# Kernel tuning notes

Hardware: AMD Instinct MI355X
Metric: run time of the kernel (lower is better)

The kernel has to match this reference:

```python
import jax, jax.numpy as jnp
import numpy as np

KRYLOV_DIM = 8
T_END = 1.0
EPS = 1e-12


def setup_inputs() -> dict:
    key = jax.random.key(0)
    k1, k2, k3 = jax.random.split(key, 3)
    B, C, H, Wd = 8, 256, 64, 64
    s0 = jax.random.uniform(k1, (B, C, H, Wd), dtype=jnp.float32)
    v = jax.random.normal(k2, (B, C, H, Wd), dtype=jnp.float32)
    W = jax.random.normal(k3, (C, C), dtype=jnp.float32) / np.float32(np.sqrt(C))
    return {"s0": s0, "v": v, "W": W}


def reference(s0, v, W):
    # fitness: learned channel-mixing linear operator (1x1-conv style)
    def fitness(x):
        return jnp.einsum('oc,bchw->bohw', W, x)

    # replicator vector field R_{s}[x] = s*x - s * sum_c(s*x)
    def replicator(s, x):
        sx = s * x
        return sx - s * jnp.sum(sx, axis=1, keepdims=True)

    A = lambda x: fitness(replicator(s0, x))
    dot = lambda a, b: jnp.sum(a * b, axis=(1, 2, 3))  # batched inner product

    m = KRYLOV_DIM
    B = v.shape[0]

    # ---- Arnoldi iteration (batched, modified Gram-Schmidt) ----
    vnorm = jnp.sqrt(dot(v, v))  # [B]
    Q = [v / vnorm[:, None, None, None]]
    Hcols = []
    for k in range(m):
        w = A(Q[k])
        col = []
        for j in range(k + 1):
            h = dot(Q[j], w)               # [B]
            col.append(h)
            w = w - h[:, None, None, None] * Q[j]
        hnext = jnp.sqrt(dot(w, w))        # subdiagonal entry
        Q.append(w / (hnext + EPS)[:, None, None, None])
        col.append(hnext)
        col += [jnp.zeros_like(hnext)] * (m - k - 1)  # pad column to m+1 rows
        Hcols.append(jnp.stack(col, axis=-1))          # [B, m+1]
    Hmat = jnp.stack(Hcols, axis=-1)  # [B, m+1, m]
    T = Hmat[:, :m, :]                # square upper-Hessenberg [B, m, m]

    # ---- extended matrix + batched small matrix exponential ----
    ext = jnp.zeros((B, m + 1, m + 1), dtype=T.dtype)
    ext = ext.at[:, :m, :m].set(T_END * T)
    ext = ext.at[:, 0, m].set(T_END)
    expm_ext = jax.scipy.linalg.expm(ext)   # batched over leading dim
    coords = expm_ext[:, :m, -1]            # [B, m] Krylov coordinates

    # ---- fused weighted sum of Krylov vectors ----
    Qstack = jnp.stack(Q[:m], axis=0)       # [m, B, C, H, W]
    v_end = jnp.einsum('bj,jbchw->bchw', coords, Qstack)
    return v_end * vnorm[:, None, None, None]
```

## Files before the change

### kernel.cpp

```cpp
#include <hip/hip_runtime.h>
#include <math.h>

#define Bn   8
#define Cn   256
#define HWn  4096
#define FB   (Cn * HWn)
#define NTOT (Bn * FB)
#define TEND 1.0
#define EPSK 1e-12f
#define NT   32
#define TPB  128
#define TSZ  8192
#define RS   40
#define WTS  36

typedef float f32x4 __attribute__((ext_vector_type(4)));
typedef short bf16x8 __attribute__((ext_vector_type(8)));

__device__ inline float b2f(unsigned int u) {
    return __uint_as_float(u << 16);
}
__device__ inline unsigned short f2b(float f) {
    unsigned u = __float_as_uint(f);
    unsigned r = u + 0x7FFFu + ((u >> 16) & 1u);
    return (unsigned short)(r >> 16);
}


__global__ void init_kernel(float* __restrict__ p) {
    for (int i = threadIdx.x; i < 1024; i += 256) p[i] = 0.0f;
}

__global__ void wsplit_kernel(const float* __restrict__ W,
                              unsigned short* __restrict__ Whs,
                              unsigned short* __restrict__ Wls) {
    int kc = blockIdx.x, mt = blockIdx.y, l = threadIdx.x;
    int m = mt * 16 + (l & 15);
    int k0 = kc * 32 + (l >> 4) * 8;
#pragma unroll
    for (int j = 0; j < 8; ++j) {
        float wv = W[m * 256 + k0 + j];
        unsigned short h = f2b(wv);
        unsigned short lo = f2b(wv - b2f(h));
        int idx = ((kc * 16 + mt) * 64 + l) * 8 + j;
        Whs[idx] = h; Wls[idx] = lo;
    }
}

template <int K>
__global__ __launch_bounds__(256, 2) void step_kernel(
        const float* __restrict__ v, const float* __restrict__ s0,
        const unsigned short* __restrict__ Whs, const unsigned short* __restrict__ Wls,
        unsigned short* __restrict__ Qb, float* __restrict__ acc,
        float* __restrict__ w) {
    __shared__ __align__(16) char smem_u[36864];
    short* Ph0 = (short*)smem_u;
    short* Ph1 = (short*)(smem_u + 2560);
    short* Pl0 = (short*)(smem_u + 5120);
    short* Pl1 = (short*)(smem_u + 7680);
    float* tredf = (float*)(smem_u + 10240);
    float* wt    = (float*)smem_u;
    __shared__ float ts[NT];
    __shared__ float nred[4];
    __shared__ float dred[4][8];

    const int tid = threadIdx.x;
    const int lane = tid & 63, wvi = tid >> 6;
    const int b = blockIdx.y;
    const int tIdx = blockIdx.x;
    const int sbase = tIdx * NT;
    const size_t boff = (size_t)b * FB;
    const size_t tb = ((size_t)b * TPB + tIdx) * TSZ;
    const int mbase = wvi * 64;
    const int cch = tid >> 3;
    const int pos4 = (tid & 7) * 4;
    const int codd = cch & 1;
    const int c2s = cch >> 1;

    float cj[K > 0 ? K : 1];
    if (K > 0) {
        float mm[K > 0 ? K : 1];
        mm[0] = sqrtf(acc[512 + b]);
#pragma unroll
        for (int j = 1; j < K; ++j) mm[j] = sqrtf(acc[512 + j * 8 + b]) + EPSK * mm[j - 1];
#pragma unroll
        for (int j = 0; j < K; ++j)
            cj[j] = acc[((K - 1) * 8 + j) * 8 + b] / (mm[j] * mm[j]);
    }
    unsigned short* QK = Qb + (size_t)(K > 0 ? K - 1 : 0) * NTOT;

    float tp[4] = {0.f, 0.f, 0.f, 0.f};
    float np = 0.f;
    for (int kc = 0; kc < 8; ++kc) {
        const size_t os = boff + (size_t)(kc * 32 + cch) * HWn + sbase + pos4;
        const size_t ot = tb + (size_t)((kc * 32 + cch) * NT + pos4);
        float4 s4 = *(const float4*)(s0 + os);
        float se[4] = {s4.x, s4.y, s4.z, s4.w};
        float xr[4];
        if (K == 0) {
            float4 x4 = *(const float4*)(v + os);
            xr[0] = x4.x; xr[1] = x4.y; xr[2] = x4.z; xr[3] = x4.w;
        } else {
            float4 w4 = *(const float4*)(w + ot);
            float4 v4 = *(const float4*)(v + os);
            float xe[4];
            xe[0] = fmaf(-cj[0], v4.x, w4.x);
            xe[1] = fmaf(-cj[0], v4.y, w4.y);
            xe[2] = fmaf(-cj[0], v4.z, w4.z);
            xe[3] = fmaf(-cj[0], v4.w, w4.w);
#pragma unroll
            for (int j = 1; j < K; ++j) {
                ushort4 u = *(const ushort4*)(Qb + (size_t)(j - 1) * NTOT + ot);
                xe[0] = fmaf(-cj[j], b2f(u.x), xe[0]);
                xe[1] = fmaf(-cj[j], b2f(u.y), xe[1]);
                xe[2] = fmaf(-cj[j], b2f(u.z), xe[2]);
                xe[3] = fmaf(-cj[j], b2f(u.w), xe[3]);
            }
            unsigned h0 = f2b(xe[0]), h1 = f2b(xe[1]);
            unsigned h2 = f2b(xe[2]), h3 = f2b(xe[3]);
            ushort4 o;
            o.x = (unsigned short)h0; o.y = (unsigned short)h1;
            o.z = (unsigned short)h2; o.w = (unsigned short)h3;
            *(ushort4*)(QK + ot) = o;
            xr[0] = b2f(h0); xr[1] = b2f(h1); xr[2] = b2f(h2); xr[3] = b2f(h3);
        }
#pragma unroll
        for (int i = 0; i < 4; ++i) {
            np = fmaf(xr[i], xr[i], np);
            tp[i] = fmaf(xr[i], se[i], tp[i]);
        }
    }
    *(float4*)(tredf + cch * WTS + pos4) = *(float4*)tp;
    {
        float q2 = np;
        for (int off2 = 32; off2 > 0; off2 >>= 1) q2 += __shfl_down(q2, off2);
        if (lane == 0) nred[wvi] = q2;
    }
    __syncthreads();
    if (tid < NT) {
        float s = 0.f;
#pragma unroll
        for (int g = 0; g < 32; ++g) s += tredf[g * WTS + tid];
        ts[tid] = s;
    }
    if (tid == 0)
        atomicAdd(&acc[512 + K * 8 + b], nred[0] + nred[1] + nred[2] + nred[3]);
    __syncthreads();

    auto wr2 = [&](short* buf, unsigned x01, unsigned x23) {
        unsigned p01 = (unsigned)__shfl_xor((int)x01, 8);
        unsigned p23 = (unsigned)__shfl_xor((int)x23, 8);
        unsigned mine = codd ? x23 : x01;
        unsigned theirs = codd ? p23 : p01;
        unsigned w0, w1;
        if (codd) {
            w0 = (theirs & 0xFFFFu) | (mine << 16);
            w1 = (theirs >> 16) | (mine & 0xFFFF0000u);
        } else {
            w0 = (mine & 0xFFFFu) | (theirs << 16);
            w1 = (mine >> 16) | (theirs & 0xFFFF0000u);
        }
        int P0 = pos4 + 2 * codd;
        int slot = c2s ^ (((P0 >> 3) & 3) << 2);
        *(unsigned*)(buf + P0 * RS + slot * 2) = w0;
        *(unsigned*)(buf + (P0 + 1) * RS + slot * 2) = w1;
    };

    auto stage = [&](int kc, int bb) {
        const size_t os = boff + (size_t)(kc * 32 + cch) * HWn + sbase + pos4;
        const size_t ot = tb + (size_t)((kc * 32 + cch) * NT + pos4);
        float4 s4 = *(const float4*)(s0 + os);
        float se[4] = {s4.x, s4.y, s4.z, s4.w};
        float xr[4];
        if (K == 0) {
            float4 x4 = *(const float4*)(v + os);
            xr[0] = x4.x; xr[1] = x4.y; xr[2] = x4.z; xr[3] = x4.w;
        } else {
            ushort4 u = *(const ushort4*)(QK + ot);
            xr[0] = b2f(u.x); xr[1] = b2f(u.y); xr[2] = b2f(u.z); xr[3] = b2f(u.w);
        }
        unsigned phx[4], plx[4];
#pragma unroll
        for (int i = 0; i < 4; ++i) {
            float pe = se[i] * (xr[i] - ts[pos4 + i]);
            unsigned hp = f2b(pe);
            phx[i] = hp; plx[i] = f2b(pe - b2f((unsigned short)hp));
        }
        wr2(bb ? Ph1 : Ph0, phx[0] | (phx[1] << 16), phx[2] | (phx[3] << 16));
        wr2(bb ? Pl1 : Pl0, plx[0] | (plx[1] << 16), plx[2] | (plx[3] << 16));
    };

    f32x4 ac[4][2];
#pragma unroll
    for (int i = 0; i < 4; ++i)
#pragma unroll
        for (int j = 0; j < 2; ++j) ac[i][j] = (f32x4){0.f, 0.f, 0.f, 0.f};

    const int r15 = lane & 15, qq = lane >> 4;
    stage(0, 0);
    for (int kc = 0; kc < 8; ++kc) {
        __syncthreads();
        bf16x8 ah[4], al[4];
#pragma unroll
        for (int rt = 0; rt < 4; ++rt) {
            int mt = wvi * 4 + rt;
            ah[rt] = *(const bf16x8*)(Whs + (size_t)kc * 8192 + (mt * 64 + lane) * 8);
            al[rt] = *(const bf16x8*)(Wls + (size_t)kc * 8192 + (mt * 64 + lane) * 8);
        }
        if (kc < 7) stage(kc + 1, (kc + 1) & 1);
        const short* ph = (kc & 1) ? Ph1 : Ph0;
        const short* pl = (kc & 1) ? Pl1 : Pl0;
#pragma unroll
        for (int ct = 0; ct < 2; ++ct) {
            int n = ct * 16 + r15;
            int grp = qq ^ ((n >> 3) & 3);
            int off = n * RS + grp * 8;
            bf16x8 bh = *(const bf16x8*)(ph + off);
            bf16x8 bl = *(const bf16x8*)(pl + off);
#pragma unroll
            for (int rt = 0; rt < 4; ++rt) {
                ac[rt][ct] = __builtin_amdgcn_mfma_f32_16x16x32_bf16(ah[rt], bh, ac[rt][ct], 0, 0, 0);
                ac[rt][ct] = __builtin_amdgcn_mfma_f32_16x16x32_bf16(ah[rt], bl, ac[rt][ct], 0, 0, 0);
                ac[rt][ct] = __builtin_amdgcn_mfma_f32_16x16x32_bf16(al[rt], bh, ac[rt][ct], 0, 0, 0);
            }
        }
    }

    __syncthreads();
#pragma unroll
    for (int rt = 0; rt < 4; ++rt)
#pragma unroll
        for (int ct = 0; ct < 2; ++ct) {
            int col = ct * 16 + r15;
            int r0 = mbase + rt * 16 + qq * 4;
#pragma unroll
            for (int reg = 0; reg < 4; ++reg)
                wt[(r0 + reg) * WTS + col] = ac[rt][ct][reg];
        }
    __syncthreads();

    float dp[K + 1];
#pragma unroll
    for (int j = 0; j <= K; ++j) dp[j] = 0.f;
#pragma unroll
    for (int rr = 0; rr < 8; ++rr) {
        int row = rr * 32 + (tid >> 3);
        int col = (tid & 7) * 4;
        float4 wf = *(const float4*)(wt + row * WTS + col);
        size_t it = tb + (size_t)(row * NT + col);
        size_t is = boff + (size_t)row * HWn + sbase + col;
        *(float4*)(w + it) = wf;
        float4 vv4 = *(const float4*)(v + is);
        dp[0] = fmaf(wf.x, vv4.x, dp[0]);
        dp[0] = fmaf(wf.y, vv4.y, dp[0]);
        dp[0] = fmaf(wf.z, vv4.z, dp[0]);
        dp[0] = fmaf(wf.w, vv4.w, dp[0]);
#pragma unroll
        for (int j = 1; j <= K; ++j) {
            ushort4 u = *(const ushort4*)(Qb + (size_t)(j - 1) * NTOT + it);
            dp[j] = fmaf(wf.x, b2f(u.x), dp[j]);
            dp[j] = fmaf(wf.y, b2f(u.y), dp[j]);
            dp[j] = fmaf(wf.z, b2f(u.z), dp[j]);
            dp[j] = fmaf(wf.w, b2f(u.w), dp[j]);
        }
    }
#pragma unroll
    for (int j = 0; j <= K; ++j) {
        float q2 = dp[j];
        for (int off2 = 32; off2 > 0; off2 >>= 1) q2 += __shfl_down(q2, off2);
        if (lane == 0) dred[wvi][j] = q2;
    }
    __syncthreads();
    if (tid <= K)
        atomicAdd(&acc[(K * 8 + tid) * 8 + b],
                  dred[0][tid] + dred[1][tid] + dred[2][tid] + dred[3][tid]);
}

__global__ __launch_bounds__(128) void expm_kernel(const float* __restrict__ acc,
                                                   float* __restrict__ coordsOut) {
    __shared__ double Am[81], Pm[81], Tm[81];
    __shared__ double ssc;
    __shared__ int sn;
    const int b = blockIdx.x;
    const int t = threadIdx.x;
    const int r = t / 9, c = t % 9;
    double m[8];
    m[0] = sqrt((double)acc[512 + b]);
    for (int j = 1; j < 8; ++j) m[j] = sqrt((double)acc[512 + j * 8 + b]) + 1e-12 * m[j - 1];
    if (t < 81) {
        double val = 0.0;
        if (r < 8 && c < 8) {
            if (r <= c) val = TEND * (double)acc[(c * 8 + r) * 8 + b] / (m[r] * m[c]);
            else if (r == c + 1) val = TEND * sqrt((double)acc[512 + r * 8 + b]) / m[c];
        }
        if (r == 0 && c == 8) val = TEND;
        Am[t] = val;
    }
    __syncthreads();
    if (t == 0) {
        double mx = 0.0;
        for (int rr = 0; rr < 9; ++rr) {
            double s = 0.0;
            for (int cc = 0; cc < 9; ++cc) s += fabs(Am[rr * 9 + cc]);
            if (s > mx) mx = s;
        }
        int n = 0;
        while (mx > 0.25 && n < 48) { mx *= 0.5; ++n; }
        double sc = 1.0;
        for (int ii = 0; ii < n; ++ii) sc *= 0.5;
        sn = n; ssc = sc;
    }
    __syncthreads();
    if (t < 81) Am[t] *= ssc;
    __syncthreads();
    if (t < 81) Pm[t] = (r == c) ? 1.0 : 0.0;
    __syncthreads();
    for (int i = 20; i >= 1; --i) {
        if (t < 81) {
            double s = 0.0;
            for (int k = 0; k < 9; ++k) s += Am[r * 9 + k] * Pm[k * 9 + c];
            Tm[t] = ((r == c) ? 1.0 : 0.0) + s / (double)i;
        }
        __syncthreads();
        if (t < 81) Pm[t] = Tm[t];
        __syncthreads();
    }
    int n = sn;
    for (int q = 0; q < n; ++q) {
        if (t < 81) {
            double s = 0.0;
            for (int k = 0; k < 9; ++k) s += Pm[r * 9 + k] * Pm[k * 9 + c];
            Tm[t] = s;
        }
        __syncthreads();
        if (t < 81) Pm[t] = Tm[t];
        __syncthreads();
    }
    if (t < 8) coordsOut[b * 8 + t] = (float)(Pm[t * 9 + 8] * m[0] / m[t]);
}

__global__ __launch_bounds__(256) void combine_kernel(const unsigned short* __restrict__ Qb,
                                                      const float* __restrict__ v,
                                                      const float* __restrict__ coords,
                                                      float* __restrict__ out) {
    int t = blockIdx.x, b = blockIdx.y;
    const size_t boff = (size_t)b * FB;
    const size_t tb = ((size_t)b * TPB + t) * TSZ;
    float cf[8];
#pragma unroll
    for (int j = 0; j < 8; ++j) cf[j] = coords[b * 8 + j];
    int rg = threadIdx.x >> 3;
    int pos4 = (threadIdx.x & 7) * 4;
#pragma unroll
    for (int ri = 0; ri < 8; ++ri) {
        int r = ri * 32 + rg;
        size_t it = tb + (size_t)(r * NT + pos4);
        size_t is = boff + (size_t)r * HWn + t * NT + pos4;
        float4 vv = *(const float4*)(v + is);
        float a[4] = {cf[0] * vv.x, cf[0] * vv.y, cf[0] * vv.z, cf[0] * vv.w};
#pragma unroll
        for (int j = 1; j < 8; ++j) {
            ushort4 u = *(const ushort4*)(Qb + (size_t)(j - 1) * NTOT + it);
            a[0] = fmaf(cf[j], b2f(u.x), a[0]);
            a[1] = fmaf(cf[j], b2f(u.y), a[1]);
            a[2] = fmaf(cf[j], b2f(u.z), a[2]);
            a[3] = fmaf(cf[j], b2f(u.w), a[3]);
        }
        float4 o = {a[0], a[1], a[2], a[3]};
        *(float4*)(out + is) = o;
    }
}

extern "C" void kernel_launch(void* const* d_in, const int* in_sizes, int n_in,
                              void* d_out, int out_size, void* d_ws, size_t ws_size,
                              hipStream_t stream) {
    const float* s0 = (const float*)d_in[0];
    const float* v  = (const float*)d_in[1];
    const float* W  = (const float*)d_in[2];
    float* out = (float*)d_out;

    float* ws     = (float*)d_ws;
    float* acc    = ws;
    float* coords = ws + 576;
    unsigned short* Whs = (unsigned short*)(ws + 1024);
    unsigned short* Wls = Whs + 65536;
    unsigned short* Qb  = (unsigned short*)(ws + 1024 + 65536);
    float* w      = out;

    init_kernel<<<dim3(1), dim3(256), 0, stream>>>(ws);
    wsplit_kernel<<<dim3(8, 16), dim3(64), 0, stream>>>(W, Whs, Wls);

    dim3 ga(TPB, 8), blk(256);
#define STEPK(K) step_kernel<K><<<ga, blk, 0, stream>>>(v, s0, Whs, Wls, Qb, acc, w);
    STEPK(0) STEPK(1) STEPK(2) STEPK(3) STEPK(4) STEPK(5) STEPK(6) STEPK(7)
#undef STEPK

    expm_kernel<<<dim3(8), dim3(128), 0, stream>>>(acc, coords);
    combine_kernel<<<dim3(TPB, 8), blk, 0, stream>>>(Qb, v, coords, out);
}
```

Baseline: 510.9 us.

## Fold replicator mean subtraction into GEMM via linearity to drop pre-pass

The step kernel no longer makes a separate pass over all channels to compute the per-pixel sum of s*x before the GEMM. It uses W(s*(x - t)) = W(s*x) - t*W(s) and computes both W(s*x) and W(s) with split-bf16 MFMAs in the same pipelined loop, applying the correction at the end. This removes one full read of the tile (s0 plus Q or v) and a barrier phase. In exchange it doubles the MFMA work and the LDS staging, uses more shared memory and accumulator registers, and may lose precision through cancellation.

New measurement: 501.5 us (median of 2 runs). About the same (-1.8%).

```diff
diff --git a/kernel.cpp b/kernel.cpp
--- a/kernel.cpp
+++ b/kernel.cpp
@@ -58,7 +58,11 @@
     short* Ph1 = (short*)(smem_u + 2560);
     short* Pl0 = (short*)(smem_u + 5120);
     short* Pl1 = (short*)(smem_u + 7680);
-    float* tredf = (float*)(smem_u + 10240);
+    short* Sh0 = (short*)(smem_u + 10240);
+    short* Sh1 = (short*)(smem_u + 12800);
+    short* Sl0 = (short*)(smem_u + 15360);
+    short* Sl1 = (short*)(smem_u + 17920);
+    float* tredf = (float*)(smem_u + 20480);
     float* wt    = (float*)smem_u;
     __shared__ float ts[NT];
     __shared__ float nred[4];
@@ -91,7 +95,27 @@
 
     float tp[4] = {0.f, 0.f, 0.f, 0.f};
     float np = 0.f;
-    for (int kc = 0; kc < 8; ++kc) {
+
+    auto wr2 = [&](short* buf, unsigned x01, unsigned x23) {
+        unsigned p01 = (unsigned)__shfl_xor((int)x01, 8);
+        unsigned p23 = (unsigned)__shfl_xor((int)x23, 8);
+        unsigned mine = codd ? x23 : x01;
+        unsigned theirs = codd ? p23 : p01;
+        unsigned w0, w1;
+        if (codd) {
+            w0 = (theirs & 0xFFFFu) | (mine << 16);
+            w1 = (theirs >> 16) | (mine & 0xFFFF0000u);
+        } else {
+            w0 = (mine & 0xFFFFu) | (theirs << 16);
+            w1 = (mine >> 16) | (theirs & 0xFFFF0000u);
+        }
+        int P0 = pos4 + 2 * codd;
+        int slot = c2s ^ (((P0 >> 3) & 3) << 2);
+        *(unsigned*)(buf + P0 * RS + slot * 2) = w0;
+        *(unsigned*)(buf + (P0 + 1) * RS + slot * 2) = w1;
+    };
+
+    auto stage = [&](int kc, int bb) {
         const size_t os = boff + (size_t)(kc * 32 + cch) * HWn + sbase + pos4;
         const size_t ot = tb + (size_t)((kc * 32 + cch) * NT + pos4);
         float4 s4 = *(const float4*)(s0 + os);
@@ -124,77 +148,31 @@
             *(ushort4*)(QK + ot) = o;
             xr[0] = b2f(h0); xr[1] = b2f(h1); xr[2] = b2f(h2); xr[3] = b2f(h3);
         }
+        unsigned phx[4], plx[4], shx[4], slx[4];
 #pragma unroll
         for (int i = 0; i < 4; ++i) {
             np = fmaf(xr[i], xr[i], np);
             tp[i] = fmaf(xr[i], se[i], tp[i]);
-        }
-    }
-    *(float4*)(tredf + cch * WTS + pos4) = *(float4*)tp;
-    {
-        float q2 = np;
-        for (int off2 = 32; off2 > 0; off2 >>= 1) q2 += __shfl_down(q2, off2);
-        if (lane == 0) nred[wvi] = q2;
-    }
-    __syncthreads();
-    if (tid < NT) {
-        float s = 0.f;
-#pragma unroll
-        for (int g = 0; g < 32; ++g) s += tredf[g * WTS + tid];
-        ts[tid] = s;
-    }
-    if (tid == 0)
-        atomicAdd(&acc[512 + K * 8 + b], nred[0] + nred[1] + nred[2] + nred[3]);
-    __syncthreads();
-
-    auto wr2 = [&](short* buf, unsigned x01, unsigned x23) {
-        unsigned p01 = (unsigned)__shfl_xor((int)x01, 8);
-        unsigned p23 = (unsigned)__shfl_xor((int)x23, 8);
-        unsigned mine = codd ? x23 : x01;
-        unsigned theirs = codd ? p23 : p01;
-        unsigned w0, w1;
-        if (codd) {
-            w0 = (theirs & 0xFFFFu) | (mine << 16);
-            w1 = (theirs >> 16) | (mine & 0xFFFF0000u);
-        } else {
-            w0 = (mine & 0xFFFFu) | (theirs << 16);
-            w1 = (mine >> 16) | (theirs & 0xFFFF0000u);
-        }
-        int P0 = pos4 + 2 * codd;
-        int slot = c2s ^ (((P0 >> 3) & 3) << 2);
-        *(unsigned*)(buf + P0 * RS + slot * 2) = w0;
-        *(unsigned*)(buf + (P0 + 1) * RS + slot * 2) = w1;
-    };
-
-    auto stage = [&](int kc, int bb) {
-        const size_t os = boff + (size_t)(kc * 32 + cch) * HWn + sbase + pos4;
-        const size_t ot = tb + (size_t)((kc * 32 + cch) * NT + pos4);
-        float4 s4 = *(const float4*)(s0 + os);
-        float se[4] = {s4.x, s4.y, s4.z, s4.w};
-        float xr[4];
-        if (K == 0) {
-            float4 x4 = *(const float4*)(v + os);
-            xr[0] = x4.x; xr[1] = x4.y; xr[2] = x4.z; xr[3] = x4.w;
-        } else {
-            ushort4 u = *(const ushort4*)(QK + ot);
-            xr[0] = b2f(u.x); xr[1] = b2f(u.y); xr[2] = b2f(u.z); xr[3] = b2f(u.w);
-        }
-        unsigned phx[4], plx[4];
-#pragma unroll
-        for (int i = 0; i < 4; ++i) {
-            float pe = se[i] * (xr[i] - ts[pos4 + i]);
+            float pe = se[i] * xr[i];
             unsigned hp = f2b(pe);
             phx[i] = hp; plx[i] = f2b(pe - b2f((unsigned short)hp));
+            unsigned hs = f2b(se[i]);
+            shx[i] = hs; slx[i] = f2b(se[i] - b2f((unsigned short)hs));
         }
         wr2(bb ? Ph1 : Ph0, phx[0] | (phx[1] << 16), phx[2] | (phx[3] << 16));
         wr2(bb ? Pl1 : Pl0, plx[0] | (plx[1] << 16), plx[2] | (plx[3] << 16));
+        wr2(bb ? Sh1 : Sh0, shx[0] | (shx[1] << 16), shx[2] | (shx[3] << 16));
+        wr2(bb ? Sl1 : Sl0, slx[0] | (slx[1] << 16), slx[2] | (slx[3] << 16));
     };
 
-    f32x4 ac[4][2];
+    f32x4 ac[4][2], az[4][2];
 #pragma unroll
     for (int i = 0; i < 4; ++i)
 #pragma unroll
-        for (int j = 0; j < 2; ++j) ac[i][j] = (f32x4){0.f, 0.f, 0.f, 0.f};
+        for (int j = 0; j < 2; ++j) {
+            ac[i][j] = (f32x4){0.f, 0.f, 0.f, 0.f};
+            az[i][j] = (f32x4){0.f, 0.f, 0.f, 0.f};
+        }
 
     const int r15 = lane & 15, qq = lane >> 4;
     stage(0, 0);
@@ -210,6 +188,8 @@
         if (kc < 7) stage(kc + 1, (kc + 1) & 1);
         const short* ph = (kc & 1) ? Ph1 : Ph0;
         const short* pl = (kc & 1) ? Pl1 : Pl0;
+        const short* sh = (kc & 1) ? Sh1 : Sh0;
+        const short* sl = (kc & 1) ? Sl1 : Sl0;
 #pragma unroll
         for (int ct = 0; ct < 2; ++ct) {
             int n = ct * 16 + r15;
@@ -217,25 +197,48 @@
             int off = n * RS + grp * 8;
             bf16x8 bh = *(const bf16x8*)(ph + off);
             bf16x8 bl = *(const bf16x8*)(pl + off);
+            bf16x8 svh = *(const bf16x8*)(sh + off);
+            bf16x8 svl = *(const bf16x8*)(sl + off);
 #pragma unroll
             for (int rt = 0; rt < 4; ++rt) {
                 ac[rt][ct] = __builtin_amdgcn_mfma_f32_16x16x32_bf16(ah[rt], bh, ac[rt][ct], 0, 0, 0);
                 ac[rt][ct] = __builtin_amdgcn_mfma_f32_16x16x32_bf16(ah[rt], bl, ac[rt][ct], 0, 0, 0);
                 ac[rt][ct] = __builtin_amdgcn_mfma_f32_16x16x32_bf16(al[rt], bh, ac[rt][ct], 0, 0, 0);
+                az[rt][ct] = __builtin_amdgcn_mfma_f32_16x16x32_bf16(ah[rt], svh, az[rt][ct], 0, 0, 0);
+                az[rt][ct] = __builtin_amdgcn_mfma_f32_16x16x32_bf16(ah[rt], svl, az[rt][ct], 0, 0, 0);
+                az[rt][ct] = __builtin_amdgcn_mfma_f32_16x16x32_bf16(al[rt], svh, az[rt][ct], 0, 0, 0);
             }
         }
     }
 
     __syncthreads();
+    *(float4*)(tredf + cch * WTS + pos4) = *(float4*)tp;
+    {
+        float q2 = np;
+        for (int off2 = 32; off2 > 0; off2 >>= 1) q2 += __shfl_down(q2, off2);
+        if (lane == 0) nred[wvi] = q2;
+    }
+    __syncthreads();
+    if (tid < NT) {
+        float s = 0.f;
+#pragma unroll
+        for (int g = 0; g < 32; ++g) s += tredf[g * WTS + tid];
+        ts[tid] = s;
+    }
+    if (tid == 0)
+        atomicAdd(&acc[512 + K * 8 + b], nred[0] + nred[1] + nred[2] + nred[3]);
+    __syncthreads();
+
 #pragma unroll
     for (int rt = 0; rt < 4; ++rt)
 #pragma unroll
         for (int ct = 0; ct < 2; ++ct) {
             int col = ct * 16 + r15;
             int r0 = mbase + rt * 16 + qq * 4;
+            float tv = ts[col];
 #pragma unroll
             for (int reg = 0; reg < 4; ++reg)
-                wt[(r0 + reg) * WTS + col] = ac[rt][ct][reg];
+                wt[(r0 + reg) * WTS + col] = ac[rt][ct][reg] - az[rt][ct][reg] * tv;
         }
     __syncthreads();
 
```
